# Performance work log

Hardware: AMD Instinct MI355X
Metric: run time of the kernel (lower is better)

## Reference

```python
import jax, jax.numpy as jnp
import numpy as np

N = 100000
E = 1600000
D = 128      # in_features
H = 128      # mlp hidden = out_features
O = 128      # out_features
BN_EPS = 1e-5

def _bn_train(x, gamma, beta):
    # BatchNorm1d in training mode: batch stats over node axis, biased variance
    mu = jnp.mean(x, axis=0)
    var = jnp.mean((x - mu) ** 2, axis=0)
    return (x - mu) * jax.lax.rsqrt(var + BN_EPS) * gamma + beta

def setup_inputs() -> dict:
    key = jax.random.key(0)
    ks = jax.random.split(key, 8)
    h = jax.random.normal(ks[0], (N, D), dtype=jnp.float32)
    edge_src = jax.random.randint(ks[1], (E,), 0, N, dtype=jnp.int32)
    edge_dst = jax.random.randint(ks[2], (E,), 0, N, dtype=jnp.int32)
    s1 = 1.0 / np.sqrt(D)
    s2 = 1.0 / np.sqrt(H)
    W1 = jax.random.uniform(ks[3], (D, H), jnp.float32, -s1, s1)
    b1 = jax.random.uniform(ks[4], (H,), jnp.float32, -s1, s1)
    W2 = jax.random.uniform(ks[5], (H, O), jnp.float32, -s2, s2)
    b2 = jax.random.uniform(ks[6], (O,), jnp.float32, -s2, s2)
    return {
        "h": h, "edge_src": edge_src, "edge_dst": edge_dst,
        "W1": W1, "b1": b1, "g1": jnp.ones((H,), jnp.float32), "be1": jnp.zeros((H,), jnp.float32),
        "W2": W2, "b2": b2, "g2": jnp.ones((O,), jnp.float32), "be2": jnp.zeros((O,), jnp.float32),
        "eps": jnp.zeros((), jnp.float32),
    }

def reference(h, edge_src, edge_dst, W1, b1, g1, be1, W2, b2, g2, be2, eps):
    # spmm(Adj, h) == scatter-add of gathered neighbor features
    msgs = h[edge_src]                                   # [E, D] irregular gather
    pooled = jax.ops.segment_sum(msgs, edge_dst, num_segments=N)  # [N, D]
    pooled = pooled + (1.0 + eps) * h                    # eps combine
    # MLP (2 layers): Linear -> BN -> ReLU -> Linear
    x = jax.nn.relu(_bn_train(pooled @ W1 + b1, g1, be1))
    x = x @ W2 + b2
    # final BN + ReLU
    return jax.nn.relu(_bn_train(x, g2, be2))
```

## Files before the change

### kernel.cpp

```cpp
#include <hip/hip_runtime.h>
#include <hip/hip_bf16.h>
#include <stdint.h>

#define BN_EPS 1e-5f
#define NSTRIPE 64

typedef __attribute__((ext_vector_type(8)))  short bf16x8;
typedef __attribute__((ext_vector_type(16))) float f32x16;

static __device__ __forceinline__ float bflo2f(uint32_t p){
  union { uint32_t u; float f; } c; c.u = p << 16; return c.f;
}
static __device__ __forceinline__ float bfhi2f(uint32_t p){
  union { uint32_t u; float f; } c; c.u = p & 0xffff0000u; return c.f;
}
static __device__ __forceinline__ uint16_t f2bf(float f){
  union { float f; uint32_t u; } c; c.f = f;
  uint32_t u = c.u;
  return (uint16_t)((u + 0x7fffu + ((u >> 16) & 1u)) >> 16);
}
static __device__ __forceinline__ uint32_t pack2(float a, float b){
  return (uint32_t)f2bf(a) | ((uint32_t)f2bf(b) << 16);
}

__global__ void k_prep(const float* __restrict__ h, uint16_t* __restrict__ hb, int hblocks,
                       const float* __restrict__ W1, const float* __restrict__ W2,
                       uint16_t* __restrict__ Wt1, uint16_t* __restrict__ Wt2,
                       float* __restrict__ stats,
                       const int* __restrict__ dst, int* __restrict__ M, int E, int NB){
  int b = blockIdx.x, t = threadIdx.x;
  if (b < hblocks){
    int i = (b * 256 + t) * 8;
    float4 a = *(const float4*)(h + i);
    float4 bb = *(const float4*)(h + i + 4);
    uint4 o;
    o.x = pack2(a.x, a.y); o.y = pack2(a.z, a.w);
    o.z = pack2(bb.x, bb.y); o.w = pack2(bb.z, bb.w);
    *(uint4*)(hb + i) = o;
    return;
  }
  if (b < hblocks + 16){
    int gid = (b - hblocks) * 256 + t;
    {
      float4 z = make_float4(0.f, 0.f, 0.f, 0.f);
      *(float4*)(stats + gid * 8) = z;
      *(float4*)(stats + gid * 8 + 4) = z;
    }
    const float* Wf = (gid < 2048) ? W1 : W2;
    uint16_t* Wt = (gid < 2048) ? Wt1 : Wt2;
    int cid = gid & 2047;
    int nrow = cid >> 4;
    int c    = cid & 15;
    int k0 = c * 8;
    float e[8];
    #pragma unroll
    for (int j = 0; j < 8; ++j) e[j] = Wf[(k0 + j) * 128 + nrow];
    uint4 o;
    o.x = pack2(e[0], e[1]); o.y = pack2(e[2], e[3]);
    o.z = pack2(e[4], e[5]); o.w = pack2(e[6], e[7]);
    *(uint4*)(Wt + nrow * 128 + c * 8) = o;
    return;
  }
  int eb = b - hblocks - 16;
  __shared__ int cnt[512];
  cnt[t] = 0; cnt[t + 256] = 0;
  __syncthreads();
  int base = eb * 4096;
  #pragma unroll 4
  for (int j = t; j < 4096; j += 256){
    int i = base + j;
    if (i < E) atomicAdd(&cnt[dst[i] >> 8], 1);
  }
  __syncthreads();
  size_t row = (size_t)eb * NB;
  if (t < NB) M[row + t] = cnt[t];
  int t2 = t + 256;
  if (t2 < NB) M[row + t2] = cnt[t2];
}

__global__ void k_colscan(int* __restrict__ M, int* __restrict__ btot, int EB, int NB){
  __shared__ int s[256];
  int b = blockIdx.x, t = threadIdx.x;
  int i0 = 2 * t, i1 = 2 * t + 1;
  int v0 = (i0 < EB) ? M[(size_t)i0 * NB + b] : 0;
  int v1 = (i1 < EB) ? M[(size_t)i1 * NB + b] : 0;
  s[t] = v0 + v1;
  __syncthreads();
  for (int off = 1; off < 256; off <<= 1){
    int v = (t >= off) ? s[t - off] : 0;
    __syncthreads();
    s[t] += v;
    __syncthreads();
  }
  int excl = s[t] - (v0 + v1);
  if (i0 < EB) M[(size_t)i0 * NB + b] = excl;
  if (i1 < EB) M[(size_t)i1 * NB + b] = excl + v0;
  if (t == 255) btot[b] = s[255];
}

__global__ void k_bscan(const int* __restrict__ btot, int* __restrict__ bbase,
                        int* __restrict__ row_off, int NB, int n, int E){
  __shared__ int s[256];
  int t = threadIdx.x;
  int i0 = 2 * t, i1 = 2 * t + 1;
  int v0 = (i0 < NB) ? btot[i0] : 0;
  int v1 = (i1 < NB) ? btot[i1] : 0;
  s[t] = v0 + v1;
  __syncthreads();
  for (int off = 1; off < 256; off <<= 1){
    int v = (t >= off) ? s[t - off] : 0;
    __syncthreads();
    s[t] += v;
    __syncthreads();
  }
  int excl = s[t] - (v0 + v1);
  if (i0 < NB) bbase[i0] = excl;
  if (i1 < NB) bbase[i1] = excl + v0;
  if (t == 0){ bbase[NB] = E; row_off[n] = E; }
}

__global__ void k_bin(const int* __restrict__ src, const int* __restrict__ dst,
                      const int* __restrict__ M, const int* __restrict__ bbase,
                      uint32_t* __restrict__ binned, int E, int NB){
  __shared__ int comb[512];
  __shared__ int cur[512];
  int t = threadIdx.x;
  size_t row = (size_t)blockIdx.x * NB;
  if (t < NB) comb[t] = bbase[t] + M[row + t];
  int t2 = t + 256;
  if (t2 < NB) comb[t2] = bbase[t2] + M[row + t2];
  cur[t] = 0; cur[t + 256] = 0;
  __syncthreads();
  int base = blockIdx.x * 4096;
  #pragma unroll 4
  for (int j = t; j < 4096; j += 256){
    int i = base + j;
    if (i < E){
      int d = dst[i];
      int b = d >> 8;
      int r = atomicAdd(&cur[b], 1);
      binned[comb[b] + r] = (uint32_t)src[i] | ((uint32_t)(d & 255) << 24);
    }
  }
}

__global__ void k_csr(const uint32_t* __restrict__ binned, const int* __restrict__ bbase,
                      int* __restrict__ row_off, int* __restrict__ col_idx, int n){
  __shared__ int cnt[256];
  __shared__ int off[256];
  __shared__ int cur[256];
  int b = blockIdx.x, t = threadIdx.x;
  int e0 = bbase[b], e1 = bbase[b + 1];
  int nb0 = b << 8;
  cnt[t] = 0; cur[t] = 0;
  __syncthreads();
  int m = e1 - e0;
  for (int j = t; j < m; j += 256) atomicAdd(&cnt[binned[e0 + j] >> 24], 1);
  __syncthreads();
  int v = cnt[t];
  off[t] = v;
  __syncthreads();
  for (int o = 1; o < 256; o <<= 1){
    int u = (t >= o) ? off[t - o] : 0;
    __syncthreads();
    off[t] += u;
    __syncthreads();
  }
  int excl = off[t] - v;
  __syncthreads();
  off[t] = excl;
  if (nb0 + t < n) row_off[nb0 + t] = e0 + excl;
  __syncthreads();
  for (int j = t; j < m; j += 256){
    uint32_t p = binned[e0 + j];
    int dl = (int)(p >> 24);
    int r = atomicAdd(&cur[dl], 1);
    col_idx[e0 + off[dl] + r] = (int)(p & 0xFFFFFFu);
  }
}

__global__ __launch_bounds__(256, 4) void k_gg(
    const uint16_t* __restrict__ hb, const int* __restrict__ row_off,
    const int* __restrict__ col_idx, const float* __restrict__ eps_p,
    const uint16_t* __restrict__ Wt, const float* __restrict__ bias_f,
    uint16_t* __restrict__ Yout, float* __restrict__ osum_s, float* __restrict__ osq_s, int n){
  __shared__ __align__(16) uint16_t Al[64 * 128];
  __shared__ float csum[128], csq[128];
  int tid = threadIdx.x;
  int rbase = blockIdx.x * 64;
  int stripe = blockIdx.x & (NSTRIPE - 1);
  int grp = tid >> 4;
  int c   = tid & 15;
  const uint4* hp4 = (const uint4*)hb;
  float ce = 1.0f + eps_p[0];
  if (tid < 128){ csum[tid] = 0.f; csq[tid] = 0.f; }

  for (int it = 0; it < 4; ++it){
    int m = it * 16 + grp;
    int gr = rbase + m;
    float a0=0.f,a1=0.f,a2=0.f,a3=0.f,a4=0.f,a5=0.f,a6=0.f,a7=0.f;
    if (gr < n){
      int j = row_off[gr], jend = row_off[gr + 1];
      for (; j + 8 <= jend; j += 8){
        int s[8];
        #pragma unroll
        for (int e = 0; e < 8; ++e) s[e] = col_idx[j + e];
        uint4 v[8];
        #pragma unroll
        for (int e = 0; e < 8; ++e) v[e] = hp4[(size_t)s[e] * 16 + c];
        #pragma unroll
        for (int e = 0; e < 8; ++e){
          a0 += bflo2f(v[e].x); a1 += bfhi2f(v[e].x);
          a2 += bflo2f(v[e].y); a3 += bfhi2f(v[e].y);
          a4 += bflo2f(v[e].z); a5 += bfhi2f(v[e].z);
          a6 += bflo2f(v[e].w); a7 += bfhi2f(v[e].w);
        }
      }
      if (j < jend){
        int s[8]; float wq[8];
        #pragma unroll
        for (int e = 0; e < 8; ++e){
          int jj = j + e;
          wq[e] = (jj < jend) ? 1.f : 0.f;
          s[e] = col_idx[(jj < jend) ? jj : (jend - 1)];
        }
        uint4 v[8];
        #pragma unroll
        for (int e = 0; e < 8; ++e) v[e] = hp4[(size_t)s[e] * 16 + c];
        #pragma unroll
        for (int e = 0; e < 8; ++e){
          a0 = fmaf(wq[e], bflo2f(v[e].x), a0); a1 = fmaf(wq[e], bfhi2f(v[e].x), a1);
          a2 = fmaf(wq[e], bflo2f(v[e].y), a2); a3 = fmaf(wq[e], bfhi2f(v[e].y), a3);
          a4 = fmaf(wq[e], bflo2f(v[e].z), a4); a5 = fmaf(wq[e], bfhi2f(v[e].z), a5);
          a6 = fmaf(wq[e], bflo2f(v[e].w), a6); a7 = fmaf(wq[e], bfhi2f(v[e].w), a7);
        }
      }
      uint4 vh = hp4[(size_t)gr * 16 + c];
      a0 = fmaf(ce, bflo2f(vh.x), a0); a1 = fmaf(ce, bfhi2f(vh.x), a1);
      a2 = fmaf(ce, bflo2f(vh.y), a2); a3 = fmaf(ce, bfhi2f(vh.y), a3);
      a4 = fmaf(ce, bflo2f(vh.z), a4); a5 = fmaf(ce, bfhi2f(vh.z), a5);
      a6 = fmaf(ce, bflo2f(vh.w), a6); a7 = fmaf(ce, bfhi2f(vh.w), a7);
    }
    uint4 o;
    o.x = pack2(a0, a1); o.y = pack2(a2, a3);
    o.z = pack2(a4, a5); o.w = pack2(a6, a7);
    *(uint4*)((char*)Al + m * 256 + ((c ^ (m & 15)) * 16)) = o;
  }
  __syncthreads();

  int lane = tid & 63;
  int w    = tid >> 6;
  int hi   = lane >> 5;
  int key  = lane & 15;
  int m0   = (w & 1) * 32;
  int n0   = (w >> 1) * 64;
  int mrow = m0 + (lane & 31);
  int nrow0 = n0 + (lane & 31);
  int nrow1 = nrow0 + 32;

  f32x16 acc0, acc1;
  #pragma unroll
  for (int i = 0; i < 16; ++i){ acc0[i] = 0.f; acc1[i] = 0.f; }

  const char* Ab = (const char*)Al;
  #pragma unroll
  for (int kt = 0; kt < 8; ++kt){
    int ck = 2 * kt + hi;
    bf16x8 a  = *(const bf16x8*)(Ab + mrow * 256 + ((ck ^ key) * 16));
    bf16x8 b0 = *(const bf16x8*)(Wt + nrow0 * 128 + ck * 8);
    bf16x8 b1 = *(const bf16x8*)(Wt + nrow1 * 128 + ck * 8);
    acc0 = __builtin_amdgcn_mfma_f32_32x32x16_bf16(a, b0, acc0, 0, 0, 0);
    acc1 = __builtin_amdgcn_mfma_f32_32x32x16_bf16(a, b1, acc1, 0, 0, 0);
  }
  __syncthreads();

  uint16_t* Yl = Al;
  float bias0 = bias_f[nrow0];
  float bias1 = bias_f[nrow1];
  float ps0 = 0.f, pq0 = 0.f, ps1 = 0.f, pq1 = 0.f;
  #pragma unroll
  for (int r = 0; r < 16; ++r){
    int row = m0 + (r & 3) + 8 * (r >> 2) + 4 * hi;
    bool valid = (rbase + row) < n;
    float y0 = acc0[r] + bias0;
    float y1 = acc1[r] + bias1;
    if (valid){
      ps0 += y0; pq0 += y0 * y0;
      ps1 += y1; pq1 += y1 * y1;
    }
    Yl[row * 128 + nrow0] = f2bf(y0);
    Yl[row * 128 + nrow1] = f2bf(y1);
  }
  atomicAdd(&csum[nrow0], ps0); atomicAdd(&csq[nrow0], pq0);
  atomicAdd(&csum[nrow1], ps1); atomicAdd(&csq[nrow1], pq1);
  __syncthreads();

  #pragma unroll
  for (int i = 0; i < 4; ++i){
    int id = tid + 256 * i;
    int row = id >> 4, cc = id & 15;
    int gr = rbase + row;
    if (gr < n)
      *((uint4*)Yout + (size_t)gr * 16 + cc) = *((const uint4*)Yl + id);
  }
  if (tid < 128){
    atomicAdd(&osum_s[stripe * 128 + tid], csum[tid]);
    atomicAdd(&osq_s[stripe * 128 + tid], csq[tid]);
  }
}

__global__ __launch_bounds__(256, 4) void k_mgemm2(
    const uint16_t* __restrict__ Ag, const uint16_t* __restrict__ Wt,
    const float* __restrict__ bias_f,
    const float* __restrict__ sin_s, const float* __restrict__ sqin_s,
    const float* __restrict__ gin, const float* __restrict__ bein, float invN,
    uint16_t* __restrict__ Yout, float* __restrict__ osum_s, float* __restrict__ osq_s, int n){
  __shared__ __align__(16) uint16_t Al[64 * 128];
  __shared__ float csum[128], csq[128];
  __shared__ __align__(16) float ABl[256];
  int tid = threadIdx.x;
  int rbase = blockIdx.x * 64;
  int stripe = blockIdx.x & (NSTRIPE - 1);

  if (tid < 128){
    float s = 0.f, q = 0.f;
    #pragma unroll 8
    for (int st = 0; st < NSTRIPE; ++st){
      s += sin_s[st * 128 + tid];
      q += sqin_s[st * 128 + tid];
    }
    float mu = s * invN;
    float var = q * invN - mu * mu;
    float A = gin[tid] * rsqrtf(var + BN_EPS);
    ABl[tid] = A;
    ABl[128 + tid] = bein[tid] - mu * A;
    csum[tid] = 0.f; csq[tid] = 0.f;
  }
  __syncthreads();

  #pragma unroll
  for (int i = 0; i < 4; ++i){
    int f = tid + 256 * i;
    int m = f >> 4, c = f & 15;
    int gr = rbase + m;
    uint4 v = make_uint4(0, 0, 0, 0);
    if (gr < n){
      v = *(const uint4*)(Ag + (size_t)gr * 128 + c * 8);
      int k0 = c * 8;
      float4 ka0 = *(const float4*)(ABl + k0);
      float4 ka1 = *(const float4*)(ABl + k0 + 4);
      float4 kb0 = *(const float4*)(ABl + 128 + k0);
      float4 kb1 = *(const float4*)(ABl + 128 + k0 + 4);
      float e0 = fmaxf(fmaf(bflo2f(v.x), ka0.x, kb0.x), 0.f);
      float e1 = fmaxf(fmaf(bfhi2f(v.x), ka0.y, kb0.y), 0.f);
      float e2 = fmaxf(fmaf(bflo2f(v.y), ka0.z, kb0.z), 0.f);
      float e3 = fmaxf(fmaf(bfhi2f(v.y), ka0.w, kb0.w), 0.f);
      float e4 = fmaxf(fmaf(bflo2f(v.z), ka1.x, kb1.x), 0.f);
      float e5 = fmaxf(fmaf(bfhi2f(v.z), ka1.y, kb1.y), 0.f);
      float e6 = fmaxf(fmaf(bflo2f(v.w), ka1.z, kb1.z), 0.f);
      float e7 = fmaxf(fmaf(bfhi2f(v.w), ka1.w, kb1.w), 0.f);
      v.x = pack2(e0, e1); v.y = pack2(e2, e3);
      v.z = pack2(e4, e5); v.w = pack2(e6, e7);
    }
    *(uint4*)((char*)Al + m * 256 + ((c ^ (m & 15)) * 16)) = v;
  }
  __syncthreads();

  int lane = tid & 63;
  int w    = tid >> 6;
  int hi   = lane >> 5;
  int key  = lane & 15;
  int m0   = (w & 1) * 32;
  int n0   = (w >> 1) * 64;
  int mrow = m0 + (lane & 31);
  int nrow0 = n0 + (lane & 31);
  int nrow1 = nrow0 + 32;

  f32x16 acc0, acc1;
  #pragma unroll
  for (int i = 0; i < 16; ++i){ acc0[i] = 0.f; acc1[i] = 0.f; }

  const char* Ab = (const char*)Al;
  #pragma unroll
  for (int kt = 0; kt < 8; ++kt){
    int ck = 2 * kt + hi;
    bf16x8 a  = *(const bf16x8*)(Ab + mrow * 256 + ((ck ^ key) * 16));
    bf16x8 b0 = *(const bf16x8*)(Wt + nrow0 * 128 + ck * 8);
    bf16x8 b1 = *(const bf16x8*)(Wt + nrow1 * 128 + ck * 8);
    acc0 = __builtin_amdgcn_mfma_f32_32x32x16_bf16(a, b0, acc0, 0, 0, 0);
    acc1 = __builtin_amdgcn_mfma_f32_32x32x16_bf16(a, b1, acc1, 0, 0, 0);
  }
  __syncthreads();

  uint16_t* Yl = Al;
  float bias0 = bias_f[nrow0];
  float bias1 = bias_f[nrow1];
  float ps0 = 0.f, pq0 = 0.f, ps1 = 0.f, pq1 = 0.f;
  #pragma unroll
  for (int r = 0; r < 16; ++r){
    int row = m0 + (r & 3) + 8 * (r >> 2) + 4 * hi;
    bool valid = (rbase + row) < n;
    float y0 = acc0[r] + bias0;
    float y1 = acc1[r] + bias1;
    if (valid){
      ps0 += y0; pq0 += y0 * y0;
      ps1 += y1; pq1 += y1 * y1;
    }
    Yl[row * 128 + nrow0] = f2bf(y0);
    Yl[row * 128 + nrow1] = f2bf(y1);
  }
  atomicAdd(&csum[nrow0], ps0); atomicAdd(&csq[nrow0], pq0);
  atomicAdd(&csum[nrow1], ps1); atomicAdd(&csq[nrow1], pq1);
  __syncthreads();

  #pragma unroll
  for (int i = 0; i < 4; ++i){
    int id = tid + 256 * i;
    int row = id >> 4, cc = id & 15;
    int gr = rbase + row;
    if (gr < n)
      *((uint4*)Yout + (size_t)gr * 16 + cc) = *((const uint4*)Yl + id);
  }
  if (tid < 128){
    atomicAdd(&osum_s[stripe * 128 + tid], csum[tid]);
    atomicAdd(&osq_s[stripe * 128 + tid], csq[tid]);
  }
}

__global__ void k_bncoef2(const float* __restrict__ sum_s, const float* __restrict__ sq_s,
                          const float* __restrict__ g, const float* __restrict__ be,
                          float* __restrict__ AB, float invN){
  int c = threadIdx.x;
  if (c < 128){
    float s = 0.f, q = 0.f;
    #pragma unroll 8
    for (int st = 0; st < NSTRIPE; ++st){
      s += sum_s[st * 128 + c];
      q += sq_s[st * 128 + c];
    }
    float mu = s * invN;
    float var = q * invN - mu * mu;
    float A = g[c] * rsqrtf(var + BN_EPS);
    AB[c] = A;
    AB[128 + c] = be[c] - mu * A;
  }
}

__global__ void k_final(const uint16_t* __restrict__ Y2b, const float* __restrict__ ABg,
                        float* __restrict__ out, int total){
  __shared__ __align__(16) float AB[256];
  int tid = threadIdx.x;
  if (tid < 64){
    *(float4*)(AB + tid * 4) = *(const float4*)(ABg + tid * 4);
  }
  __syncthreads();
  int i = (blockIdx.x * 256 + tid) * 4;
  if (i >= total) return;
  uint2 v = *(const uint2*)(Y2b + i);
  int c = i & 127;
  float4 a = *(const float4*)(AB + c);
  float4 b = *(const float4*)(AB + 128 + c);
  float4 o;
  o.x = fmaxf(fmaf(bflo2f(v.x), a.x, b.x), 0.f);
  o.y = fmaxf(fmaf(bfhi2f(v.x), a.y, b.y), 0.f);
  o.z = fmaxf(fmaf(bflo2f(v.y), a.z, b.z), 0.f);
  o.w = fmaxf(fmaf(bfhi2f(v.y), a.w, b.w), 0.f);
  *(float4*)(out + i) = o;
}

extern "C" void kernel_launch(void* const* d_in, const int* in_sizes, int n_in,
                              void* d_out, int out_size, void* d_ws, size_t ws_size,
                              hipStream_t stream){
  const float* h    = (const float*)d_in[0];
  const int*   esrc = (const int*)d_in[1];
  const int*   edst = (const int*)d_in[2];
  const float* W1   = (const float*)d_in[3];
  const float* b1   = (const float*)d_in[4];
  const float* g1   = (const float*)d_in[5];
  const float* be1  = (const float*)d_in[6];
  const float* W2   = (const float*)d_in[7];
  const float* b2   = (const float*)d_in[8];
  const float* g2   = (const float*)d_in[9];
  const float* be2  = (const float*)d_in[10];
  const float* eps  = (const float*)d_in[11];
  int n = in_sizes[0] / 128;
  int E = in_sizes[1];
  (void)n_in; (void)out_size; (void)ws_size;

  int NB = (n + 255) >> 8;
  int EB = (E + 4095) >> 12;

  char* ws = (char*)d_ws;
  size_t off = 0;
  auto alloc = [&](size_t bytes) -> void* {
    void* p = ws + off;
    off += (bytes + 511) & ~(size_t)511;
    return p;
  };
  size_t feat_b = (size_t)n * 128 * 2;
  uint16_t* B1   = (uint16_t*)alloc(feat_b);
  uint16_t* B2   = (uint16_t*)alloc(feat_b);
  int*   row_off = (int*)alloc((size_t)(n + 1) * 4);
  int*   col_idx = (int*)alloc((size_t)E * 4);
  int*   M       = (int*)alloc((size_t)EB * NB * 4);
  int*   btot    = (int*)alloc((size_t)(NB + 1) * 4);
  int*   bbase   = (int*)alloc((size_t)(NB + 1) * 4);
  float* stats   = (float*)alloc((size_t)4 * NSTRIPE * 128 * 4);
  float* AB2     = (float*)alloc(256 * 4);
  uint16_t* Wt1  = (uint16_t*)alloc(128 * 128 * 2);
  uint16_t* Wt2  = (uint16_t*)alloc(128 * 128 * 2);
  float* sum1 = stats;
  float* sq1  = stats + NSTRIPE * 128;
  float* sum2 = stats + 2 * NSTRIPE * 128;
  float* sq2  = stats + 3 * NSTRIPE * 128;
  uint16_t* hb  = B1;
  uint32_t* binned = (uint32_t*)B2;
  uint16_t* Y1b = B2;
  uint16_t* Y2b = B1;

  int total = n * 128;
  int hblocks = total / 8 / 256;
  float invN = 1.0f / (float)n;

  k_prep<<<hblocks + 16 + EB, 256, 0, stream>>>(h, hb, hblocks, W1, W2, Wt1, Wt2,
                                                stats, edst, M, E, NB);
  k_colscan<<<NB, 256, 0, stream>>>(M, btot, EB, NB);
  k_bscan  <<<1, 256, 0, stream>>>(btot, bbase, row_off, NB, n, E);
  k_bin    <<<EB, 256, 0, stream>>>(esrc, edst, M, bbase, binned, E, NB);
  k_csr    <<<NB, 256, 0, stream>>>(binned, bbase, row_off, col_idx, n);

  int gblocks = (n + 63) / 64;
  k_gg<<<gblocks, 256, 0, stream>>>(hb, row_off, col_idx, eps, Wt1, b1,
                                    Y1b, sum1, sq1, n);
  k_mgemm2<<<gblocks, 256, 0, stream>>>(Y1b, Wt2, b2,
      sum1, sq1, g1, be1, invN, Y2b, sum2, sq2, n);

  k_bncoef2<<<1, 128, 0, stream>>>(sum2, sq2, g2, be2, AB2, invN);
  k_final<<<(total / 4 + 255) / 256, 256, 0, stream>>>(Y2b, AB2, (float*)d_out, total);
}
```

Before: 300.4 us.

## Make gather-GEMM kernels persistent with atomic tile scheduler and 32-row tiles

The gather+GEMM1 kernel and the BN+ReLU+GEMM2 kernel become persistent grids of up to 2048 blocks. Each block pulls 32-row tiles from a global atomic counter, and the counters are zeroed in the prep kernel. Tiles shrink from 64 to 32 rows, each wave computes a single 32x32 MFMA output block, and launch bounds rise to 8 blocks per CU. The aim is better load balance across irregular row degrees and higher occupancy to hide gather latency. The cost is an atomic plus an extra barrier per tile and reloading the same weight B-fragments more often per row processed.

```diff
diff --git a/kernel.cpp b/kernel.cpp
--- a/kernel.cpp
+++ b/kernel.cpp
@@ -26,7 +26,7 @@
 __global__ void k_prep(const float* __restrict__ h, uint16_t* __restrict__ hb, int hblocks,
                        const float* __restrict__ W1, const float* __restrict__ W2,
                        uint16_t* __restrict__ Wt1, uint16_t* __restrict__ Wt2,
-                       float* __restrict__ stats,
+                       float* __restrict__ stats, int* __restrict__ ctr,
                        const int* __restrict__ dst, int* __restrict__ M, int E, int NB){
   int b = blockIdx.x, t = threadIdx.x;
   if (b < hblocks){
@@ -41,6 +41,7 @@
   }
   if (b < hblocks + 16){
     int gid = (b - hblocks) * 256 + t;
+    if (gid == 0){ ctr[0] = 0; ctr[1] = 0; }
     {
       float4 z = make_float4(0.f, 0.f, 0.f, 0.f);
       *(float4*)(stats + gid * 8) = z;
@@ -179,148 +180,144 @@
   }
 }
 
-__global__ __launch_bounds__(256, 4) void k_gg(
+__global__ __launch_bounds__(256, 8) void k_gg(
     const uint16_t* __restrict__ hb, const int* __restrict__ row_off,
     const int* __restrict__ col_idx, const float* __restrict__ eps_p,
     const uint16_t* __restrict__ Wt, const float* __restrict__ bias_f,
-    uint16_t* __restrict__ Yout, float* __restrict__ osum_s, float* __restrict__ osq_s, int n){
-  __shared__ __align__(16) uint16_t Al[64 * 128];
+    uint16_t* __restrict__ Yout, float* __restrict__ osum_s, float* __restrict__ osq_s,
+    int* __restrict__ ctr, int ntiles, int n){
+  __shared__ __align__(16) uint16_t Al[32 * 128];
   __shared__ float csum[128], csq[128];
+  __shared__ int tile_s;
   int tid = threadIdx.x;
-  int rbase = blockIdx.x * 64;
-  int stripe = blockIdx.x & (NSTRIPE - 1);
   int grp = tid >> 4;
   int c   = tid & 15;
   const uint4* hp4 = (const uint4*)hb;
   float ce = 1.0f + eps_p[0];
-  if (tid < 128){ csum[tid] = 0.f; csq[tid] = 0.f; }
-
-  for (int it = 0; it < 4; ++it){
-    int m = it * 16 + grp;
-    int gr = rbase + m;
-    float a0=0.f,a1=0.f,a2=0.f,a3=0.f,a4=0.f,a5=0.f,a6=0.f,a7=0.f;
-    if (gr < n){
-      int j = row_off[gr], jend = row_off[gr + 1];
-      for (; j + 8 <= jend; j += 8){
-        int s[8];
-        #pragma unroll
-        for (int e = 0; e < 8; ++e) s[e] = col_idx[j + e];
-        uint4 v[8];
-        #pragma unroll
-        for (int e = 0; e < 8; ++e) v[e] = hp4[(size_t)s[e] * 16 + c];
-        #pragma unroll
-        for (int e = 0; e < 8; ++e){
-          a0 += bflo2f(v[e].x); a1 += bfhi2f(v[e].x);
-          a2 += bflo2f(v[e].y); a3 += bfhi2f(v[e].y);
-          a4 += bflo2f(v[e].z); a5 += bfhi2f(v[e].z);
-          a6 += bflo2f(v[e].w); a7 += bfhi2f(v[e].w);
-        }
-      }
-      if (j < jend){
-        int s[8]; float wq[8];
-        #pragma unroll
-        for (int e = 0; e < 8; ++e){
-          int jj = j + e;
-          wq[e] = (jj < jend) ? 1.f : 0.f;
-          s[e] = col_idx[(jj < jend) ? jj : (jend - 1)];
-        }
-        uint4 v[8];
-        #pragma unroll
-        for (int e = 0; e < 8; ++e) v[e] = hp4[(size_t)s[e] * 16 + c];
-        #pragma unroll
-        for (int e = 0; e < 8; ++e){
-          a0 = fmaf(wq[e], bflo2f(v[e].x), a0); a1 = fmaf(wq[e], bfhi2f(v[e].x), a1);
-          a2 = fmaf(wq[e], bflo2f(v[e].y), a2); a3 = fmaf(wq[e], bfhi2f(v[e].y), a3);
-          a4 = fmaf(wq[e], bflo2f(v[e].z), a4); a5 = fmaf(wq[e], bfhi2f(v[e].z), a5);
-          a6 = fmaf(wq[e], bflo2f(v[e].w), a6); a7 = fmaf(wq[e], bfhi2f(v[e].w), a7);
-        }
-      }
-      uint4 vh = hp4[(size_t)gr * 16 + c];
-      a0 = fmaf(ce, bflo2f(vh.x), a0); a1 = fmaf(ce, bfhi2f(vh.x), a1);
-      a2 = fmaf(ce, bflo2f(vh.y), a2); a3 = fmaf(ce, bfhi2f(vh.y), a3);
-      a4 = fmaf(ce, bflo2f(vh.z), a4); a5 = fmaf(ce, bfhi2f(vh.z), a5);
-      a6 = fmaf(ce, bflo2f(vh.w), a6); a7 = fmaf(ce, bfhi2f(vh.w), a7);
-    }
-    uint4 o;
-    o.x = pack2(a0, a1); o.y = pack2(a2, a3);
-    o.z = pack2(a4, a5); o.w = pack2(a6, a7);
-    *(uint4*)((char*)Al + m * 256 + ((c ^ (m & 15)) * 16)) = o;
-  }
-  __syncthreads();
 
   int lane = tid & 63;
   int w    = tid >> 6;
   int hi   = lane >> 5;
   int key  = lane & 15;
-  int m0   = (w & 1) * 32;
-  int n0   = (w >> 1) * 64;
-  int mrow = m0 + (lane & 31);
-  int nrow0 = n0 + (lane & 31);
-  int nrow1 = nrow0 + 32;
-
-  f32x16 acc0, acc1;
-  #pragma unroll
-  for (int i = 0; i < 16; ++i){ acc0[i] = 0.f; acc1[i] = 0.f; }
-
-  const char* Ab = (const char*)Al;
-  #pragma unroll
-  for (int kt = 0; kt < 8; ++kt){
-    int ck = 2 * kt + hi;
-    bf16x8 a  = *(const bf16x8*)(Ab + mrow * 256 + ((ck ^ key) * 16));
-    bf16x8 b0 = *(const bf16x8*)(Wt + nrow0 * 128 + ck * 8);
-    bf16x8 b1 = *(const bf16x8*)(Wt + nrow1 * 128 + ck * 8);
-    acc0 = __builtin_amdgcn_mfma_f32_32x32x16_bf16(a, b0, acc0, 0, 0, 0);
-    acc1 = __builtin_amdgcn_mfma_f32_32x32x16_bf16(a, b1, acc1, 0, 0, 0);
-  }
-  __syncthreads();
-
-  uint16_t* Yl = Al;
+  int mrow = lane & 31;
+  int nrow0 = w * 32 + (lane & 31);
   float bias0 = bias_f[nrow0];
-  float bias1 = bias_f[nrow1];
-  float ps0 = 0.f, pq0 = 0.f, ps1 = 0.f, pq1 = 0.f;
-  #pragma unroll
-  for (int r = 0; r < 16; ++r){
-    int row = m0 + (r & 3) + 8 * (r >> 2) + 4 * hi;
-    bool valid = (rbase + row) < n;
-    float y0 = acc0[r] + bias0;
-    float y1 = acc1[r] + bias1;
-    if (valid){
-      ps0 += y0; pq0 += y0 * y0;
-      ps1 += y1; pq1 += y1 * y1;
-    }
-    Yl[row * 128 + nrow0] = f2bf(y0);
-    Yl[row * 128 + nrow1] = f2bf(y1);
-  }
-  atomicAdd(&csum[nrow0], ps0); atomicAdd(&csq[nrow0], pq0);
-  atomicAdd(&csum[nrow1], ps1); atomicAdd(&csq[nrow1], pq1);
-  __syncthreads();
-
-  #pragma unroll
-  for (int i = 0; i < 4; ++i){
-    int id = tid + 256 * i;
-    int row = id >> 4, cc = id & 15;
-    int gr = rbase + row;
-    if (gr < n)
-      *((uint4*)Yout + (size_t)gr * 16 + cc) = *((const uint4*)Yl + id);
-  }
-  if (tid < 128){
-    atomicAdd(&osum_s[stripe * 128 + tid], csum[tid]);
-    atomicAdd(&osq_s[stripe * 128 + tid], csq[tid]);
-  }
-}
-
-__global__ __launch_bounds__(256, 4) void k_mgemm2(
+
+  while (true){
+    if (tid == 0) tile_s = atomicAdd(ctr, 1);
+    __syncthreads();
+    int tile = tile_s;
+    if (tile >= ntiles) break;
+    int rbase = tile * 32;
+    int stripe = tile & (NSTRIPE - 1);
+    if (tid < 128){ csum[tid] = 0.f; csq[tid] = 0.f; }
+
+    for (int it = 0; it < 2; ++it){
+      int m = it * 16 + grp;
+      int gr = rbase + m;
+      float a0=0.f,a1=0.f,a2=0.f,a3=0.f,a4=0.f,a5=0.f,a6=0.f,a7=0.f;
+      if (gr < n){
+        int j = row_off[gr], jend = row_off[gr + 1];
+        for (; j + 8 <= jend; j += 8){
+          int s[8];
+          #pragma unroll
+          for (int e = 0; e < 8; ++e) s[e] = col_idx[j + e];
+          uint4 v[8];
+          #pragma unroll
+          for (int e = 0; e < 8; ++e) v[e] = hp4[(size_t)s[e] * 16 + c];
+          #pragma unroll
+          for (int e = 0; e < 8; ++e){
+            a0 += bflo2f(v[e].x); a1 += bfhi2f(v[e].x);
+            a2 += bflo2f(v[e].y); a3 += bfhi2f(v[e].y);
+            a4 += bflo2f(v[e].z); a5 += bfhi2f(v[e].z);
+            a6 += bflo2f(v[e].w); a7 += bfhi2f(v[e].w);
+          }
+        }
+        if (j < jend){
+          int s[8]; float wq[8];
+          #pragma unroll
+          for (int e = 0; e < 8; ++e){
+            int jj = j + e;
+            wq[e] = (jj < jend) ? 1.f : 0.f;
+            s[e] = col_idx[(jj < jend) ? jj : (jend - 1)];
+          }
+          uint4 v[8];
+          #pragma unroll
+          for (int e = 0; e < 8; ++e) v[e] = hp4[(size_t)s[e] * 16 + c];
+          #pragma unroll
+          for (int e = 0; e < 8; ++e){
+            a0 = fmaf(wq[e], bflo2f(v[e].x), a0); a1 = fmaf(wq[e], bfhi2f(v[e].x), a1);
+            a2 = fmaf(wq[e], bflo2f(v[e].y), a2); a3 = fmaf(wq[e], bfhi2f(v[e].y), a3);
+            a4 = fmaf(wq[e], bflo2f(v[e].z), a4); a5 = fmaf(wq[e], bfhi2f(v[e].z), a5);
+            a6 = fmaf(wq[e], bflo2f(v[e].w), a6); a7 = fmaf(wq[e], bfhi2f(v[e].w), a7);
+          }
+        }
+        uint4 vh = hp4[(size_t)gr * 16 + c];
+        a0 = fmaf(ce, bflo2f(vh.x), a0); a1 = fmaf(ce, bfhi2f(vh.x), a1);
+        a2 = fmaf(ce, bflo2f(vh.y), a2); a3 = fmaf(ce, bfhi2f(vh.y), a3);
+        a4 = fmaf(ce, bflo2f(vh.z), a4); a5 = fmaf(ce, bfhi2f(vh.z), a5);
+        a6 = fmaf(ce, bflo2f(vh.w), a6); a7 = fmaf(ce, bfhi2f(vh.w), a7);
+      }
+      uint4 o;
+      o.x = pack2(a0, a1); o.y = pack2(a2, a3);
+      o.z = pack2(a4, a5); o.w = pack2(a6, a7);
+      *(uint4*)((char*)Al + m * 256 + ((c ^ (m & 15)) * 16)) = o;
+    }
+    __syncthreads();
+
+    f32x16 acc;
+    #pragma unroll
+    for (int i = 0; i < 16; ++i) acc[i] = 0.f;
+    const char* Ab = (const char*)Al;
+    #pragma unroll
+    for (int kt = 0; kt < 8; ++kt){
+      int ck = 2 * kt + hi;
+      bf16x8 a  = *(const bf16x8*)(Ab + mrow * 256 + ((ck ^ key) * 16));
+      bf16x8 b0 = *(const bf16x8*)(Wt + nrow0 * 128 + ck * 8);
+      acc = __builtin_amdgcn_mfma_f32_32x32x16_bf16(a, b0, acc, 0, 0, 0);
+    }
+    __syncthreads();
+
+    uint16_t* Yl = Al;
+    float ps0 = 0.f, pq0 = 0.f;
+    #pragma unroll
+    for (int r = 0; r < 16; ++r){
+      int row = (r & 3) + 8 * (r >> 2) + 4 * hi;
+      bool valid = (rbase + row) < n;
+      float y0 = acc[r] + bias0;
+      if (valid){ ps0 += y0; pq0 += y0 * y0; }
+      Yl[row * 128 + nrow0] = f2bf(y0);
+    }
+    atomicAdd(&csum[nrow0], ps0); atomicAdd(&csq[nrow0], pq0);
+    __syncthreads();
+
+    #pragma unroll
+    for (int i = 0; i < 2; ++i){
+      int id = tid + 256 * i;
+      int row = id >> 4, cc = id & 15;
+      int gr = rbase + row;
+      if (gr < n)
+        *((uint4*)Yout + (size_t)gr * 16 + cc) = *((const uint4*)Yl + id);
+    }
+    if (tid < 128){
+      atomicAdd(&osum_s[stripe * 128 + tid], csum[tid]);
+      atomicAdd(&osq_s[stripe * 128 + tid], csq[tid]);
+    }
+  }
+}
+
+__global__ __launch_bounds__(256, 8) void k_mgemm2(
     const uint16_t* __restrict__ Ag, const uint16_t* __restrict__ Wt,
     const float* __restrict__ bias_f,
     const float* __restrict__ sin_s, const float* __restrict__ sqin_s,
     const float* __restrict__ gin, const float* __restrict__ bein, float invN,
-    uint16_t* __restrict__ Yout, float* __restrict__ osum_s, float* __restrict__ osq_s, int n){
-  __shared__ __align__(16) uint16_t Al[64 * 128];
+    uint16_t* __restrict__ Yout, float* __restrict__ osum_s, float* __restrict__ osq_s,
+    int* __restrict__ ctr, int ntiles, int n){
+  __shared__ __align__(16) uint16_t Al[32 * 128];
   __shared__ float csum[128], csq[128];
   __shared__ __align__(16) float ABl[256];
+  __shared__ int tile_s;
   int tid = threadIdx.x;
-  int rbase = blockIdx.x * 64;
-  int stripe = blockIdx.x & (NSTRIPE - 1);
 
   if (tid < 128){
     float s = 0.f, q = 0.f;
@@ -334,96 +331,91 @@
     float A = gin[tid] * rsqrtf(var + BN_EPS);
     ABl[tid] = A;
     ABl[128 + tid] = bein[tid] - mu * A;
-    csum[tid] = 0.f; csq[tid] = 0.f;
-  }
-  __syncthreads();
-
-  #pragma unroll
-  for (int i = 0; i < 4; ++i){
-    int f = tid + 256 * i;
-    int m = f >> 4, c = f & 15;
-    int gr = rbase + m;
-    uint4 v = make_uint4(0, 0, 0, 0);
-    if (gr < n){
-      v = *(const uint4*)(Ag + (size_t)gr * 128 + c * 8);
-      int k0 = c * 8;
-      float4 ka0 = *(const float4*)(ABl + k0);
-      float4 ka1 = *(const float4*)(ABl + k0 + 4);
-      float4 kb0 = *(const float4*)(ABl + 128 + k0);
-      float4 kb1 = *(const float4*)(ABl + 128 + k0 + 4);
-      float e0 = fmaxf(fmaf(bflo2f(v.x), ka0.x, kb0.x), 0.f);
-      float e1 = fmaxf(fmaf(bfhi2f(v.x), ka0.y, kb0.y), 0.f);
-      float e2 = fmaxf(fmaf(bflo2f(v.y), ka0.z, kb0.z), 0.f);
-      float e3 = fmaxf(fmaf(bfhi2f(v.y), ka0.w, kb0.w), 0.f);
-      float e4 = fmaxf(fmaf(bflo2f(v.z), ka1.x, kb1.x), 0.f);
-      float e5 = fmaxf(fmaf(bfhi2f(v.z), ka1.y, kb1.y), 0.f);
-      float e6 = fmaxf(fmaf(bflo2f(v.w), ka1.z, kb1.z), 0.f);
-      float e7 = fmaxf(fmaf(bfhi2f(v.w), ka1.w, kb1.w), 0.f);
-      v.x = pack2(e0, e1); v.y = pack2(e2, e3);
-      v.z = pack2(e4, e5); v.w = pack2(e6, e7);
-    }
-    *(uint4*)((char*)Al + m * 256 + ((c ^ (m & 15)) * 16)) = v;
-  }
-  __syncthreads();
+  }
 
   int lane = tid & 63;
   int w    = tid >> 6;
   int hi   = lane >> 5;
   int key  = lane & 15;
-  int m0   = (w & 1) * 32;
-  int n0   = (w >> 1) * 64;
-  int mrow = m0 + (lane & 31);
-  int nrow0 = n0 + (lane & 31);
-  int nrow1 = nrow0 + 32;
-
-  f32x16 acc0, acc1;
-  #pragma unroll
-  for (int i = 0; i < 16; ++i){ acc0[i] = 0.f; acc1[i] = 0.f; }
-
-  const char* Ab = (const char*)Al;
-  #pragma unroll
-  for (int kt = 0; kt < 8; ++kt){
-    int ck = 2 * kt + hi;
-    bf16x8 a  = *(const bf16x8*)(Ab + mrow * 256 + ((ck ^ key) * 16));
-    bf16x8 b0 = *(const bf16x8*)(Wt + nrow0 * 128 + ck * 8);
-    bf16x8 b1 = *(const bf16x8*)(Wt + nrow1 * 128 + ck * 8);
-    acc0 = __builtin_amdgcn_mfma_f32_32x32x16_bf16(a, b0, acc0, 0, 0, 0);
-    acc1 = __builtin_amdgcn_mfma_f32_32x32x16_bf16(a, b1, acc1, 0, 0, 0);
-  }
-  __syncthreads();
-
-  uint16_t* Yl = Al;
+  int mrow = lane & 31;
+  int nrow0 = w * 32 + (lane & 31);
   float bias0 = bias_f[nrow0];
-  float bias1 = bias_f[nrow1];
-  float ps0 = 0.f, pq0 = 0.f, ps1 = 0.f, pq1 = 0.f;
-  #pragma unroll
-  for (int r = 0; r < 16; ++r){
-    int row = m0 + (r & 3) + 8 * (r >> 2) + 4 * hi;
-    bool valid = (rbase + row) < n;
-    float y0 = acc0[r] + bias0;
-    float y1 = acc1[r] + bias1;
-    if (valid){
-      ps0 += y0; pq0 += y0 * y0;
-      ps1 += y1; pq1 += y1 * y1;
-    }
-    Yl[row * 128 + nrow0] = f2bf(y0);
-    Yl[row * 128 + nrow1] = f2bf(y1);
-  }
-  atomicAdd(&csum[nrow0], ps0); atomicAdd(&csq[nrow0], pq0);
-  atomicAdd(&csum[nrow1], ps1); atomicAdd(&csq[nrow1], pq1);
-  __syncthreads();
-
-  #pragma unroll
-  for (int i = 0; i < 4; ++i){
-    int id = tid + 256 * i;
-    int row = id >> 4, cc = id & 15;
-    int gr = rbase + row;
-    if (gr < n)
-      *((uint4*)Yout + (size_t)gr * 16 + cc) = *((const uint4*)Yl + id);
-  }
-  if (tid < 128){
-    atomicAdd(&osum_s[stripe * 128 + tid], csum[tid]);
-    atomicAdd(&osq_s[stripe * 128 + tid], csq[tid]);
+
+  while (true){
+    if (tid == 0) tile_s = atomicAdd(ctr, 1);
+    __syncthreads();
+    int tile = tile_s;
+    if (tile >= ntiles) break;
+    int rbase = tile * 32;
+    int stripe = tile & (NSTRIPE - 1);
+    if (tid < 128){ csum[tid] = 0.f; csq[tid] = 0.f; }
+
+    #pragma unroll
+    for (int i = 0; i < 2; ++i){
+      int f = tid + 256 * i;
+      int m = f >> 4, c = f & 15;
+      int gr = rbase + m;
+      uint4 v = make_uint4(0, 0, 0, 0);
+      if (gr < n){
+        v = *(const uint4*)(Ag + (size_t)gr * 128 + c * 8);
+        int k0 = c * 8;
+        float4 ka0 = *(const float4*)(ABl + k0);
+        float4 ka1 = *(const float4*)(ABl + k0 + 4);
+        float4 kb0 = *(const float4*)(ABl + 128 + k0);
+        float4 kb1 = *(const float4*)(ABl + 128 + k0 + 4);
+        float e0 = fmaxf(fmaf(bflo2f(v.x), ka0.x, kb0.x), 0.f);
+        float e1 = fmaxf(fmaf(bfhi2f(v.x), ka0.y, kb0.y), 0.f);
+        float e2 = fmaxf(fmaf(bflo2f(v.y), ka0.z, kb0.z), 0.f);
+        float e3 = fmaxf(fmaf(bfhi2f(v.y), ka0.w, kb0.w), 0.f);
+        float e4 = fmaxf(fmaf(bflo2f(v.z), ka1.x, kb1.x), 0.f);
+        float e5 = fmaxf(fmaf(bfhi2f(v.z), ka1.y, kb1.y), 0.f);
+        float e6 = fmaxf(fmaf(bflo2f(v.w), ka1.z, kb1.z), 0.f);
+        float e7 = fmaxf(fmaf(bfhi2f(v.w), ka1.w, kb1.w), 0.f);
+        v.x = pack2(e0, e1); v.y = pack2(e2, e3);
+        v.z = pack2(e4, e5); v.w = pack2(e6, e7);
+      }
+      *(uint4*)((char*)Al + m * 256 + ((c ^ (m & 15)) * 16)) = v;
+    }
+    __syncthreads();
+
+    f32x16 acc;
+    #pragma unroll
+    for (int i = 0; i < 16; ++i) acc[i] = 0.f;
+    const char* Ab = (const char*)Al;
+    #pragma unroll
+    for (int kt = 0; kt < 8; ++kt){
+      int ck = 2 * kt + hi;
+      bf16x8 a  = *(const bf16x8*)(Ab + mrow * 256 + ((ck ^ key) * 16));
+      bf16x8 b0 = *(const bf16x8*)(Wt + nrow0 * 128 + ck * 8);
+      acc = __builtin_amdgcn_mfma_f32_32x32x16_bf16(a, b0, acc, 0, 0, 0);
+    }
+    __syncthreads();
+
+    uint16_t* Yl = Al;
+    float ps0 = 0.f, pq0 = 0.f;
+    #pragma unroll
+    for (int r = 0; r < 16; ++r){
+      int row = (r & 3) + 8 * (r >> 2) + 4 * hi;
+      bool valid = (rbase + row) < n;
+      float y0 = acc[r] + bias0;
+      if (valid){ ps0 += y0; pq0 += y0 * y0; }
+      Yl[row * 128 + nrow0] = f2bf(y0);
+    }
+    atomicAdd(&csum[nrow0], ps0); atomicAdd(&csq[nrow0], pq0);
+    __syncthreads();
+
+    #pragma unroll
+    for (int i = 0; i < 2; ++i){
+      int id = tid + 256 * i;
+      int row = id >> 4, cc = id & 15;
+      int gr = rbase + row;
+      if (gr < n)
+        *((uint4*)Yout + (size_t)gr * 16 + cc) = *((const uint4*)Yl + id);
+    }
+    if (tid < 128){
+      atomicAdd(&osum_s[stripe * 128 + tid], csum[tid]);
+      atomicAdd(&osq_s[stripe * 128 + tid], csq[tid]);
+    }
   }
 }
 
@@ -509,6 +501,7 @@
   float* AB2     = (float*)alloc(256 * 4);
   uint16_t* Wt1  = (uint16_t*)alloc(128 * 128 * 2);
   uint16_t* Wt2  = (uint16_t*)alloc(128 * 128 * 2);
+  int*   ctr     = (int*)alloc(8 * 4);
   float* sum1 = stats;
   float* sq1  = stats + NSTRIPE * 128;
   float* sum2 = stats + 2 * NSTRIPE * 128;
@@ -523,17 +516,18 @@
   float invN = 1.0f / (float)n;
 
   k_prep<<<hblocks + 16 + EB, 256, 0, stream>>>(h, hb, hblocks, W1, W2, Wt1, Wt2,
-                                                stats, edst, M, E, NB);
+                                                stats, ctr, edst, M, E, NB);
   k_colscan<<<NB, 256, 0, stream>>>(M, btot, EB, NB);
   k_bscan  <<<1, 256, 0, stream>>>(btot, bbase, row_off, NB, n, E);
   k_bin    <<<EB, 256, 0, stream>>>(esrc, edst, M, bbase, binned, E, NB);
   k_csr    <<<NB, 256, 0, stream>>>(binned, bbase, row_off, col_idx, n);
 
-  int gblocks = (n + 63) / 64;
-  k_gg<<<gblocks, 256, 0, stream>>>(hb, row_off, col_idx, eps, Wt1, b1,
-                                    Y1b, sum1, sq1, n);
-  k_mgemm2<<<gblocks, 256, 0, stream>>>(Y1b, Wt2, b2,
-      sum1, sq1, g1, be1, invN, Y2b, sum2, sq2, n);
+  int ntiles = (n + 31) / 32;
+  int pblocks = ntiles < 2048 ? ntiles : 2048;
+  k_gg<<<pblocks, 256, 0, stream>>>(hb, row_off, col_idx, eps, Wt1, b1,
+                                    Y1b, sum1, sq1, ctr, ntiles, n);
+  k_mgemm2<<<pblocks, 256, 0, stream>>>(Y1b, Wt2, b2,
+      sum1, sq1, g1, be1, invN, Y2b, sum2, sq2, ctr + 1, ntiles, n);
 
   k_bncoef2<<<1, 128, 0, stream>>>(sum2, sq2, g2, be2, AB2, invN);
   k_final<<<(total / 4 + 255) / 256, 256, 0, stream>>>(Y2b, AB2, (float*)d_out, total);
```

New measurement: 403.9 us. 34.5% more time.
